# Kernel tuning notes

Hardware: AMD Instinct MI355X
Metric: run time of the kernel (lower is better)

The kernel has to match this reference:

```python
import math
import jax, jax.numpy as jnp
import numpy as np

N, C, H, W = 8, 128, 112, 112
# frozen random.randint shifts from __init__
S7_01, S8_10 = 2, -1          # roll along dim1 (c), dim3 (h)
S11_11, S12_10, S12_11, S13_11 = 1, -1, 0, 1  # rolls along dim4 (w) / dim3 (h)


def _conv(x, w, padding, rhs_dilation=(1, 1), groups=1):
    return jax.lax.conv_general_dilated(
        x, w, window_strides=(1, 1), padding=padding,
        lhs_dilation=(1, 1), rhs_dilation=rhs_dilation,
        dimension_numbers=('NCHW', 'OIHW', 'NCHW'),
        feature_group_count=groups)


def setup_inputs() -> dict:
    key = jax.random.key(0)
    ks = jax.random.split(key, 6)
    x = jax.random.normal(ks[0], (N, C, H, W), jnp.float32)
    w3 = jax.random.normal(ks[1], (C, C, 1, 3), jnp.float32) * 0.02   # Conv2d(c,c,(1,3),dil=(1,2),pad=(0,2))
    w4 = jax.random.normal(ks[2], (C, 1, 7, 1), jnp.float32) * 0.02   # depthwise Conv2d(c,c,(7,1),dil=(3,1),pad=(9,0),groups=c)
    w9 = jax.random.normal(ks[3], (1, C, C), jnp.float32) * 0.02      # p_9_w
    w10 = jax.random.normal(ks[4], (1, C, 7, 1, 1), jnp.float32) * 0.02  # p_10_w
    w15 = jax.random.normal(ks[5], (C, C * 7 // 4, 1, 1), jnp.float32) * 0.02  # Conv2d(c*7,c,1,groups=4)
    return {"x": x, "w3": w3, "w4": w4, "w9": w9, "w10": w10, "w15": w15}


def reference(x, w3, w4, w9, w10, w15):
    n, c, h, w = x.shape
    hw = h * w
    t1 = jax.nn.sigmoid(x)
    t2 = t1 * x                                   # SiLU
    t3 = _conv(t2, w3, ((0, 0), (2, 2)), rhs_dilation=(1, 2))
    t4 = _conv(t3, w4, ((9, 9), (0, 0)), rhs_dilation=(3, 1), groups=c)
    # channel attention: bmm(t1, t0^T) / sqrt(h*w) -> (n,c,c)
    t5 = jnp.einsum('ncs,nds->ncd', t1.reshape(n, c, hw), x.reshape(n, c, hw)) / math.sqrt(hw)
    # F.unfold(t4, (7,1), dilation=(2,1), padding=(6,0)) -> (n,c,7,h,w)
    padded = jnp.pad(t4, ((0, 0), (0, 0), (6, 6), (0, 0)))
    t6 = jnp.stack([padded[:, :, 2 * k:2 * k + h, :] for k in range(7)], axis=2)
    t7 = jnp.roll(t6, S7_01, axis=1)
    t8 = jnp.roll(t7, S8_10, axis=3)
    t9 = w9 * t5
    t10 = w10 * t8
    t11 = jnp.roll(t10, S11_11, axis=4)
    t12 = jnp.roll(jnp.roll(t11, S12_10, axis=3), S12_11, axis=4)
    t13 = jnp.roll(t12, S13_11, axis=4)
    # bmm(t9^T, t2) / sqrt(c): out[n,d,s] = sum_c t9[n,c,d] * t2[n,c,s]
    t14 = (jnp.einsum('ncd,ncs->nds', t9, t2.reshape(n, c, hw)) / math.sqrt(c)).reshape(n, c, h, w)
    t15 = _conv(t13.reshape(n, c * 7, h, w), w15, ((0, 0), (0, 0)), groups=4)
    return t15 + t14
```

## Files before the change

kernel.cpp:

```cpp
#include <hip/hip_runtime.h>
#include <hip/hip_bf16.h>

#define NB 8
#define CC 128
#define HH 112
#define WW 112
#define HWS (HH*WW)
#define PLANE (CC*HWS)
#define TOT (NB*PLANE)
#define XP 116
#define LROW 130
#define PLANEP ((size_t)HH*XP*CC)

typedef __attribute__((ext_vector_type(8))) short short8v;
typedef __attribute__((ext_vector_type(4))) float float4v;

__device__ __forceinline__ float bflo(unsigned u){ return __uint_as_float(u<<16); }
__device__ __forceinline__ float bfhi(unsigned u){ return __uint_as_float(u & 0xffff0000u); }
__device__ __forceinline__ float ldv(const float* p, size_t i){ return p[i]; }
__device__ __forceinline__ float ldv(const ushort* p, size_t i){ return __uint_as_float(((unsigned)p[i])<<16); }
__device__ __forceinline__ void ld8(const ushort* p, float* v){
    uint4 u0 = *((const uint4*)p);
    v[0]=bflo(u0.x); v[1]=bfhi(u0.x); v[2]=bflo(u0.y); v[3]=bfhi(u0.y);
    v[4]=bflo(u0.z); v[5]=bfhi(u0.z); v[6]=bflo(u0.w); v[7]=bfhi(u0.w);
}
__device__ __forceinline__ void ld8(const float* p, float* v){
    float4 a = *((const float4*)p); float4 b = *((const float4*)(p+4));
    v[0]=a.x; v[1]=a.y; v[2]=a.z; v[3]=a.w; v[4]=b.x; v[5]=b.y; v[6]=b.z; v[7]=b.w;
}
__device__ __forceinline__ void ld4(const float* p, float* v){
    float4 a = *((const float4*)p);
    v[0]=a.x; v[1]=a.y; v[2]=a.z; v[3]=a.w;
}
__device__ __forceinline__ void ld4(const ushort* p, float* v){
    uint2 u = *((const uint2*)p);
    v[0]=bflo(u.x); v[1]=bfhi(u.x); v[2]=bflo(u.y); v[3]=bfhi(u.y);
}
__device__ __forceinline__ ushort f2bf(float f){
    unsigned u = __float_as_uint(f);
    return (ushort)((u + 0x7fffu + ((u>>16)&1u)) >> 16);
}
__device__ __forceinline__ void stv(float* o, size_t i, float v){ o[i]=v; }
__device__ __forceinline__ void stv(ushort* o, size_t i, float v){ o[i]=f2bf(v); }

__global__ __launch_bounds__(256) void detect_k(const ushort* __restrict__ x, int* __restrict__ flag){
    __shared__ int cnt;
    if (threadIdx.x==0) cnt = 0;
    __syncthreads();
    int bad = 0;
    for (int i = threadIdx.x; i < 2048; i += 256){
        float v = ldv(x, i);
        if (!(v > -1e4f && v < 1e4f)) bad++;
    }
    atomicAdd(&cnt, bad);
    __syncthreads();
    if (threadIdx.x==0) *flag = (cnt > 64) ? 1 : 0;
}

template<typename ET>
__device__ __forceinline__ void wpack_body(const ET* __restrict__ w3, ushort* __restrict__ Wpk){
    int idx = blockIdx.x*256 + threadIdx.x;
    if (idx < CC*384){
        int o = idx/384, kap = idx - o*384;
        int k = kap>>7, i = kap&127;
        Wpk[idx] = f2bf(ldv(w3, (o*128+i)*3 + k));
    }
}
__global__ __launch_bounds__(256) void wpack_k(const void* w3, ushort* Wpk, const int* fl){
    if (*fl) wpack_body((const float*)w3, Wpk); else wpack_body((const ushort*)w3, Wpk);
}

template<typename ET>
__device__ __forceinline__ void bpad_body(const ET* __restrict__ x, ushort* __restrict__ Bpad){
    int y = blockIdx.x, n = blockIdx.y;
    __shared__ ushort px[XP*LROW];
    const ET* xb = x + (size_t)n*PLANE + y*WW;
    for (int idx=threadIdx.x; idx<CC*28; idx+=256){
        int i = idx/28, xq = (idx - i*28)*4;
        float v[4]; ld4(xb + (size_t)i*HWS + xq, v);
        #pragma unroll
        for (int d=0;d<4;d++){
            float vv = v[d];
            float sv = vv * (1.f/(1.f+expf(-vv)));
            px[(xq+d+2)*LROW + i] = f2bf(sv);
        }
    }
    for (int idx=threadIdx.x; idx<4*CC; idx+=256){
        int j = idx >> 7, i = idx & 127;
        int xp = (j<2) ? j : j+112;
        px[xp*LROW + i] = 0;
    }
    __syncthreads();
    ushort* ob = Bpad + ((size_t)n*HH + y)*XP*CC;
    for (int idx=threadIdx.x; idx<XP*16; idx+=256){
        int xp = idx >> 4, c8 = idx & 15;
        const ushort* pr = px + xp*LROW + c8*8;
        uint4 v;
        v.x = *((const uint*)(pr+0));
        v.y = *((const uint*)(pr+2));
        v.z = *((const uint*)(pr+4));
        v.w = *((const uint*)(pr+6));
        *((uint4*)(ob + (size_t)xp*CC + c8*8)) = v;
    }
}
__global__ __launch_bounds__(256) void bpad_k(const void* x, ushort* Bpad, const int* fl){
    if (*fl) bpad_body((const float*)x, Bpad); else bpad_body((const ushort*)x, Bpad);
}

__global__ __launch_bounds__(256) void conv3mm_k(const ushort* __restrict__ Bpad, const ushort* __restrict__ Wpk,
                                                 ushort* __restrict__ t3T){
    int bx = blockIdx.x;
    int n  = blockIdx.y;
    int sbi = bx >> 1, oh = bx & 1;
    int wid = threadIdx.x >> 6, lane = threadIdx.x & 63;
    int l15 = lane & 15, quad = lane >> 4;
    __shared__ ushort Alds[24576];
    {
        const int tid = threadIdx.x;
        uint4 tmp[12];
        #pragma unroll
        for (int it=0; it<12; it++){
            int g = it*256 + tid;
            int kcmt = g >> 6, sl = (g>>2)&15, sq = g&3;
            int kc = kcmt >> 2, mt = kcmt & 3;
            tmp[it] = *((const uint4*)(Wpk + (size_t)(oh*64 + mt*16 + sl)*384 + kc*32 + sq*8));
        }
        #pragma unroll
        for (int it=0; it<12; it++){
            int g = it*256 + tid;
            *((uint4*)(Alds + g*8)) = tmp[it];
        }
    }
    __syncthreads();

    int s0 = sbi*128 + wid*32;
    int s1 = s0 + l15, s2 = s1 + 16;
    int y1 = s1/WW, x1 = s1 - y1*WW;
    int y2 = s2/WW, x2 = s2 - y2*WW;
    const ushort* bb = Bpad + (size_t)n*PLANEP;
    const ushort* b1p = bb + ((size_t)y1*XP + x1)*CC + quad*8;
    const ushort* b2p = bb + ((size_t)y2*XP + x2)*CC + quad*8;
    const ushort* al = Alds + l15*32 + quad*8;

    float4v acc[4][2] = {};
    short8v BA[2][4], BB[2][4], a0[4], a1[4];

    auto ldb = [&](int g, short8v (&B)[2][4]){
        #pragma unroll
        for (int m=0;m<4;m++){
            B[0][m] = *((const short8v*)(b1p + g*256 + m*32));
            B[1][m] = *((const short8v*)(b2p + g*256 + m*32));
        }
    };
    auto lda = [&](int kc, short8v (&dst)[4]){
        #pragma unroll
        for (int mt=0;mt<4;mt++) dst[mt] = *((const short8v*)(al + (kc*4+mt)*512));
    };
    auto step = [&](const short8v (&a)[4], const short8v (&B)[2][4], int m){
        #pragma unroll
        for (int mt=0;mt<4;mt++){
            acc[mt][0] = __builtin_amdgcn_mfma_f32_16x16x32_bf16(a[mt], B[0][m], acc[mt][0],0,0,0);
            acc[mt][1] = __builtin_amdgcn_mfma_f32_16x16x32_bf16(a[mt], B[1][m], acc[mt][1],0,0,0);
        }
    };

    ldb(0, BA); lda(0, a0);
    ldb(1, BB);
    lda(1, a1);  step(a0, BA, 0);
    lda(2, a0);  step(a1, BA, 1);
    lda(3, a1);  step(a0, BA, 2);
    lda(4, a0);  step(a1, BA, 3);
    ldb(2, BA);
    lda(5, a1);  step(a0, BB, 0);
    lda(6, a0);  step(a1, BB, 1);
    lda(7, a1);  step(a0, BB, 2);
    lda(8, a0);  step(a1, BB, 3);
    lda(9, a1);  step(a0, BA, 0);
    lda(10, a0); step(a1, BA, 1);
    lda(11, a1); step(a0, BA, 2);
                 step(a1, BA, 3);

    ushort* tb = t3T + (size_t)n*PLANE;
    #pragma unroll
    for (int nt=0; nt<2; nt++){
        int s = s0 + nt*16 + l15;
        ushort* rowp = tb + (size_t)s*128 + oh*64 + quad*4;
        #pragma unroll
        for (int mt=0; mt<4; mt++){
            ushort4 v;
            v.x = f2bf(acc[mt][nt][0]); v.y = f2bf(acc[mt][nt][1]);
            v.z = f2bf(acc[mt][nt][2]); v.w = f2bf(acc[mt][nt][3]);
            *((ushort4*)(rowp + mt*16)) = v;
        }
    }
}

template<typename ET>
__device__ __forceinline__ void wdpack_body(const ET* __restrict__ w4, float* __restrict__ wdp){
    int idx = blockIdx.x*256 + threadIdx.x;
    if (idx < 896){ int k = idx >> 7, c = idx & 127; wdp[idx] = ldv(w4, c*7 + k); }
}
__global__ __launch_bounds__(256) void wdpack_k(const void* w4, float* wdp, const int* fl){
    if (*fl) wdpack_body((const float*)w4, wdp); else wdpack_body((const ushort*)w4, wdp);
}

__global__ __launch_bounds__(256) void dwconvT_k(const ushort* __restrict__ t3T, const float* __restrict__ wdp,
                                                 ushort* __restrict__ t4T){
    int by = blockIdx.x, n = blockIdx.y;
    int y = (by>>3) + (by&7)*14;
    const ushort* tb = t3T + (size_t)n*PLANE;
    ushort* ob = t4T + (size_t)n*PLANE + (size_t)y*WW*128;
    for (int it = threadIdx.x; it < WW*16; it += 256){
        int c8 = it & 15, x = it >> 4;
        int coff = c8*8;
        float acc8[8] = {0.f,0.f,0.f,0.f,0.f,0.f,0.f,0.f};
        #pragma unroll
        for (int k=0;k<7;k++){
            int row = y - 9 + 3*k;
            if (row < 0 || row >= HH) continue;
            float v[8]; ld8(tb + ((size_t)row*WW + x)*128 + coff, v);
            const float* wp = wdp + k*128 + coff;
            #pragma unroll
            for (int j=0;j<8;j++) acc8[j] = fmaf(wp[j], v[j], acc8[j]);
        }
        ushort tmp[8];
        #pragma unroll
        for (int j=0;j<8;j++) tmp[j] = f2bf(acc8[j]);
        *((short8v*)(ob + (size_t)x*128 + coff)) = *((const short8v*)tmp);
    }
}

template<typename ET>
__device__ __forceinline__ void fusew_body(const ET* __restrict__ w10, const ET* __restrict__ w15,
                                           ushort* __restrict__ Wfb){
    int idx = blockIdx.x*256+threadIdx.x;
    if (idx < CC*224){
        int o = idx / 224, r = idx - o*224;
        int g = o >> 5;
        int cl = r/7, k = r - cl*7;
        int c = g*32 + cl;
        Wfb[idx] = f2bf(ldv(w15, o*224 + r) * ldv(w10, c*7+k));
    }
}
__global__ __launch_bounds__(256) void fusew_k(const void* w10, const void* w15, ushort* Wfb, const int* fl){
    if (*fl) fusew_body((const float*)w10, (const float*)w15, Wfb);
    else     fusew_body((const ushort*)w10, (const ushort*)w15, Wfb);
}

__global__ __launch_bounds__(256) void wfapack_k(const ushort* __restrict__ Wfb, ushort* __restrict__ Wfa){
    int idx = blockIdx.x*256 + threadIdx.x;
    if (idx >= 57344) return;
    int j   = idx & 31;
    int l15 = (idx >> 5) & 15;
    int mt  = (idx >> 9) & 1;
    int q   = (idx >> 10) & 1;
    int k   = (idx >> 11) % 7;
    int w   = idx / 14336;
    int o = w*32 + mt*16 + l15;
    int cl = -1;
    if (q==1){ if (j < 30) cl = j + 2; }
    else     { if (j >= 30) cl = j - 30; }
    Wfa[idx] = (cl >= 0) ? Wfb[o*224 + cl*7 + k] : (ushort)0;
}

__global__ __launch_bounds__(256) void t15v2_k(const ushort* __restrict__ t4T, const ushort* __restrict__ Wfa,
                                               ushort* __restrict__ u){
    int by = blockIdx.x, n = blockIdx.y;
    int y = (by>>3) + (by&7)*14;
    int w = threadIdx.x >> 6, lane = threadIdx.x & 63;
    int l15 = lane & 15, quad = lane >> 4;
    int qlo = (w+3)&3;
    float4v acc[7][2] = {};
    const ushort* tbase = t4T + (size_t)n*PLANE;
    for (int k=0;k<7;k++){
        int row = y + 2*k - 6;
        if (row < 0 || row >= HH) continue;
        const ushort* af = Wfa + (w*7 + k)*2048 + l15*32 + quad*8;
        short8v A00 = *((const short8v*)(af));
        short8v A01 = *((const short8v*)(af + 512));
        short8v A10 = *((const short8v*)(af + 1024));
        short8v A11 = *((const short8v*)(af + 1536));
        const ushort* rbase = tbase + ((size_t)row*WW + l15)*128 + quad*8;
        #pragma unroll
        for (int st=0; st<7; st++){
            const ushort* bp = rbase + st*16*128;
            short8v B0 = *((const short8v*)(bp + qlo*32));
            short8v B1 = *((const short8v*)(bp + w*32));
            acc[st][0] = __builtin_amdgcn_mfma_f32_16x16x32_bf16(A00, B0, acc[st][0], 0,0,0);
            acc[st][1] = __builtin_amdgcn_mfma_f32_16x16x32_bf16(A01, B0, acc[st][1], 0,0,0);
            acc[st][0] = __builtin_amdgcn_mfma_f32_16x16x32_bf16(A10, B1, acc[st][0], 0,0,0);
            acc[st][1] = __builtin_amdgcn_mfma_f32_16x16x32_bf16(A11, B1, acc[st][1], 0,0,0);
        }
    }
    ushort* ub = u + ((size_t)n*CC + w*32)*HWS + (size_t)y*WW;
    #pragma unroll
    for (int st=0; st<7; st++){
        int s = st*16 + l15;
        #pragma unroll
        for (int mt=0; mt<2; mt++)
            #pragma unroll
            for (int r=0;r<4;r++)
                ub[(size_t)(mt*16+quad*4+r)*HWS + s] = f2bf(acc[st][mt][r]);
    }
}

template<typename ET>
__device__ __forceinline__ void t5mm_body(const ET* __restrict__ x, float* __restrict__ t5){
    int ks = blockIdx.x, n = blockIdx.y;
    int wid = threadIdx.x>>6, lane = threadIdx.x&63;
    int l15 = lane&15, quad = lane>>4;
    const ET* xn = x + (size_t)n*PLANE;
    float4v acc[2][8] = {};
    for (int t=0; t<8; t++){
        int sb = ks*256 + t*32 + quad*8;
        short8v afr[2];
        #pragma unroll
        for (int mt=0; mt<2; mt++){
            int row = wid*32 + mt*16 + l15;
            float v[8]; ld8(xn + (size_t)row*HWS + sb, v);
            ushort tmp[8];
            #pragma unroll
            for (int j=0;j<8;j++) tmp[j] = f2bf(1.f/(1.f+expf(-v[j])));
            afr[mt] = *((const short8v*)tmp);
        }
        #pragma unroll
        for (int nt=0; nt<8; nt++){
            int row = nt*16 + l15;
            float v[8]; ld8(xn + (size_t)row*HWS + sb, v);
            ushort tmp[8];
            #pragma unroll
            for (int j=0;j<8;j++) tmp[j] = f2bf(v[j]);
            short8v bfr = *((const short8v*)tmp);
            acc[0][nt] = __builtin_amdgcn_mfma_f32_16x16x32_bf16(afr[0], bfr, acc[0][nt], 0,0,0);
            acc[1][nt] = __builtin_amdgcn_mfma_f32_16x16x32_bf16(afr[1], bfr, acc[1][nt], 0,0,0);
        }
    }
    float* t5n = t5 + n*16384;
    #pragma unroll
    for (int mt=0; mt<2; mt++){
        #pragma unroll
        for (int nt=0; nt<8; nt++){
            #pragma unroll
            for (int r=0; r<4; r++){
                int ci = wid*32 + mt*16 + quad*4 + r;
                int cj = nt*16 + l15;
                atomicAdd(&t5n[ci*128 + cj], acc[mt][nt][r]);
            }
        }
    }
}
__global__ __launch_bounds__(256) void t5mm_k(const void* x, float* t5, const int* fl){
    if (*fl) t5mm_body((const float*)x, t5); else t5mm_body((const ushort*)x, t5);
}

template<typename ET>
__device__ __forceinline__ void coefb_body(const ET* __restrict__ w9, const float* __restrict__ t5,
                                           ushort* __restrict__ coefb){
    const float sc = 7.89181775e-4f;
    int idx = blockIdx.x*256 + threadIdx.x;
    int n = idx >> 14, rem = idx & 16383;
    int d = rem >> 7, c = rem & 127;
    coefb[idx] = f2bf(ldv(w9, c*128 + d) * t5[n*16384 + c*128 + d] * sc);
}
__global__ __launch_bounds__(256) void coefb_k(const void* w9, const float* t5, ushort* coefb, const int* fl){
    if (*fl) coefb_body((const float*)w9, t5, coefb); else coefb_body((const ushort*)w9, t5, coefb);
}

template<typename OT>
__device__ __forceinline__ void final2_body(const ushort* __restrict__ Bpad, const ushort* __restrict__ coefb,
                                            const ushort* __restrict__ u, OT* __restrict__ out){
    int sb = blockIdx.x, n = blockIdx.y;
    int wid = threadIdx.x>>6, lane = threadIdx.x&63;
    int l15 = lane&15, quad = lane>>4;
    int shalf = wid >> 1, ohalf = wid & 1;
    int s0 = sb*64 + shalf*32;
    int s1 = s0 + l15, s2 = s1 + 16;
    int y1 = s1/WW, x1 = s1 - y1*WW;
    int y2 = s2/WW, x2 = s2 - y2*WW;
    const ushort* bb = Bpad + (size_t)n*PLANEP;
    const ushort* b1p = bb + ((size_t)y1*XP + x1 + 2)*CC + quad*8;
    const ushort* b2p = bb + ((size_t)y2*XP + x2 + 2)*CC + quad*8;
    const ushort* abase = coefb + (size_t)n*16384 + (size_t)(ohalf*64 + l15)*128 + quad*8;
    float4v acc[4][2] = {};
    short8v bv0[4], bv1[4], aP[4], aQ[4];
    #pragma unroll
    for (int kc=0;kc<4;kc++){
        bv0[kc] = *((const short8v*)(b1p + kc*32));
        bv1[kc] = *((const short8v*)(b2p + kc*32));
    }
    auto lda = [&](int kc, short8v (&dst)[4]){
        #pragma unroll
        for (int mt=0;mt<4;mt++) dst[mt] = *((const short8v*)(abase + mt*16*128 + kc*32));
    };
    auto step = [&](const short8v (&a)[4], int kc){
        #pragma unroll
        for (int mt=0;mt<4;mt++){
            acc[mt][0] = __builtin_amdgcn_mfma_f32_16x16x32_bf16(a[mt], bv0[kc], acc[mt][0],0,0,0);
            acc[mt][1] = __builtin_amdgcn_mfma_f32_16x16x32_bf16(a[mt], bv1[kc], acc[mt][1],0,0,0);
        }
    };
    lda(0, aP);
    lda(1, aQ); step(aP, 0);
    lda(2, aP); step(aQ, 1);
    lda(3, aQ); step(aP, 2);
                step(aQ, 3);
    #pragma unroll
    for (int mt=0; mt<4; mt++){
        #pragma unroll
        for (int nt=0; nt<2; nt++){
            int s = s0 + nt*16 + l15;
            int y = s/WW, xx = s - y*WW;
            int ys = y+2; if (ys>=HH) ys-=HH;
            int xs = xx-2; if (xs<0) xs+=WW;
            #pragma unroll
            for (int r=0; r<4; r++){
                int d = ohalf*64 + mt*16 + quad*4 + r;
                float val = ldv(u, ((size_t)n*CC+d)*HWS + ys*WW + xs) + acc[mt][nt][r];
                stv(out, ((size_t)n*CC+d)*HWS + s, val);
            }
        }
    }
}
__global__ __launch_bounds__(256) void final2_k(const ushort* Bpad, const ushort* coefb,
                                                const ushort* u, void* out, const int* fl){
    if (*fl) final2_body(Bpad, coefb, u, (float*)out);
    else     final2_body(Bpad, coefb, u, (ushort*)out);
}

extern "C" void kernel_launch(void* const* d_in, const int* in_sizes, int n_in,
                              void* d_out, int out_size, void* d_ws, size_t ws_size,
                              hipStream_t stream) {
    const void* x   = d_in[0];
    const void* w3  = d_in[1];
    const void* w4  = d_in[2];
    const void* w9  = d_in[3];
    const void* w10 = d_in[4];
    const void* w15 = d_in[5];

    ushort* t3T  = (ushort*)d_ws;
    ushort* u    = t3T;
    ushort* t4T  = t3T + TOT;
    ushort* Bpad = t4T + TOT;
    float*  t5   = (float*)(Bpad + NB*PLANEP);
    ushort* coefb= (ushort*)(t5 + NB*CC*CC);
    ushort* Wfb  = coefb + NB*CC*CC;
    ushort* Wpk  = Wfb + CC*224;
    ushort* Wfa  = Wpk + CC*384;
    float*  wdp  = (float*)(Wfa + 57344);
    int* flag    = (int*)(wdp + 896);

    detect_k<<<1, 256, 0, stream>>>((const ushort*)x, flag);
    hipMemsetAsync(t5, 0, NB*CC*CC*sizeof(float), stream);

    wpack_k  <<<192, 256, 0, stream>>>(w3, Wpk, flag);
    fusew_k  <<<112, 256, 0, stream>>>(w10, w15, Wfb, flag);
    wfapack_k<<<224, 256, 0, stream>>>(Wfb, Wfa);
    wdpack_k <<<4,   256, 0, stream>>>(w4, wdp, flag);
    bpad_k   <<<dim3(HH,NB), 256, 0, stream>>>(x, Bpad, flag);
    conv3mm_k<<<dim3(196,NB), 256, 0, stream>>>(Bpad, Wpk, t3T);
    dwconvT_k<<<dim3(HH,NB), 256, 0, stream>>>(t3T, wdp, t4T);
    t5mm_k   <<<dim3(49,NB), 256, 0, stream>>>(x, t5, flag);
    coefb_k  <<<NB*CC*CC/256, 256, 0, stream>>>(w9, t5, coefb, flag);
    t15v2_k  <<<dim3(HH,NB), 256, 0, stream>>>(t4T, Wfa, u);
    final2_k <<<dim3(196,NB), 256, 0, stream>>>(Bpad, coefb, u, d_out, flag);
}
```

Baseline: 328.4 us.

## Split t15 kernel over two column halves and double-buffer row loads

```diff
diff --git a/kernel.cpp b/kernel.cpp
--- a/kernel.cpp
+++ b/kernel.cpp
@@ -263,45 +263,80 @@
     Wfa[idx] = (cl >= 0) ? Wfb[o*224 + cl*7 + k] : (ushort)0;
 }
 
-__global__ __launch_bounds__(256) void t15v2_k(const ushort* __restrict__ t4T, const ushort* __restrict__ Wfa,
-                                               ushort* __restrict__ u){
-    int by = blockIdx.x, n = blockIdx.y;
-    int y = (by>>3) + (by&7)*14;
-    int w = threadIdx.x >> 6, lane = threadIdx.x & 63;
-    int l15 = lane & 15, quad = lane >> 4;
+template<int ST0, int NST>
+__device__ __forceinline__ void t15_body(const ushort* __restrict__ tbase, const ushort* __restrict__ Wfa,
+                                         ushort* __restrict__ ub, int y, int w, int l15, int quad){
     int qlo = (w+3)&3;
-    float4v acc[7][2] = {};
-    const ushort* tbase = t4T + (size_t)n*PLANE;
-    for (int k=0;k<7;k++){
+    float4v acc[NST][2] = {};
+    const ushort* xbase = tbase + ((size_t)(ST0*16) + l15)*128 + quad*8;
+
+    auto ldrow = [&](int k, short8v (&B)[NST][2]){
         int row = y + 2*k - 6;
-        if (row < 0 || row >= HH) continue;
+        const ushort* rbase = xbase + (size_t)row*WW*128;
+        #pragma unroll
+        for (int st=0; st<NST; st++){
+            const ushort* bp = rbase + st*16*128;
+            B[st][0] = *((const short8v*)(bp + qlo*32));
+            B[st][1] = *((const short8v*)(bp + w*32));
+        }
+    };
+    auto ldA = [&](int k, short8v (&A)[4]){
         const ushort* af = Wfa + (w*7 + k)*2048 + l15*32 + quad*8;
-        short8v A00 = *((const short8v*)(af));
-        short8v A01 = *((const short8v*)(af + 512));
-        short8v A10 = *((const short8v*)(af + 1024));
-        short8v A11 = *((const short8v*)(af + 1536));
-        const ushort* rbase = tbase + ((size_t)row*WW + l15)*128 + quad*8;
-        #pragma unroll
-        for (int st=0; st<7; st++){
-            const ushort* bp = rbase + st*16*128;
-            short8v B0 = *((const short8v*)(bp + qlo*32));
-            short8v B1 = *((const short8v*)(bp + w*32));
-            acc[st][0] = __builtin_amdgcn_mfma_f32_16x16x32_bf16(A00, B0, acc[st][0], 0,0,0);
-            acc[st][1] = __builtin_amdgcn_mfma_f32_16x16x32_bf16(A01, B0, acc[st][1], 0,0,0);
-            acc[st][0] = __builtin_amdgcn_mfma_f32_16x16x32_bf16(A10, B1, acc[st][0], 0,0,0);
-            acc[st][1] = __builtin_amdgcn_mfma_f32_16x16x32_bf16(A11, B1, acc[st][1], 0,0,0);
-        }
-    }
-    ushort* ub = u + ((size_t)n*CC + w*32)*HWS + (size_t)y*WW;
+        A[0] = *((const short8v*)(af));
+        A[1] = *((const short8v*)(af + 512));
+        A[2] = *((const short8v*)(af + 1024));
+        A[3] = *((const short8v*)(af + 1536));
+    };
+    auto domm = [&](const short8v (&A)[4], const short8v (&B)[NST][2]){
+        #pragma unroll
+        for (int st=0; st<NST; st++){
+            acc[st][0] = __builtin_amdgcn_mfma_f32_16x16x32_bf16(A[0], B[st][0], acc[st][0], 0,0,0);
+            acc[st][1] = __builtin_amdgcn_mfma_f32_16x16x32_bf16(A[1], B[st][0], acc[st][1], 0,0,0);
+            acc[st][0] = __builtin_amdgcn_mfma_f32_16x16x32_bf16(A[2], B[st][1], acc[st][0], 0,0,0);
+            acc[st][1] = __builtin_amdgcn_mfma_f32_16x16x32_bf16(A[3], B[st][1], acc[st][1], 0,0,0);
+        }
+    };
+
+    if (y >= 6 && y <= 105){
+        short8v BA[NST][2], BB[NST][2], A0[4], A1[4];
+        ldrow(0, BA); ldrow(1, BB);
+        ldA(0, A0);              domm(A0, BA);
+        ldrow(2, BA); ldA(1, A1); domm(A1, BB);
+        ldrow(3, BB); ldA(2, A0); domm(A0, BA);
+        ldrow(4, BA); ldA(3, A1); domm(A1, BB);
+        ldrow(5, BB); ldA(4, A0); domm(A0, BA);
+        ldrow(6, BA); ldA(5, A1); domm(A1, BB);
+                      ldA(6, A0); domm(A0, BA);
+    } else {
+        int klo = (y >= 6) ? 0 : ((7 - y) >> 1);
+        int khi = min(6, (117 - y) >> 1);
+        for (int k = klo; k <= khi; k++){
+            short8v B[NST][2], A[4];
+            ldrow(k, B); ldA(k, A); domm(A, B);
+        }
+    }
+
     #pragma unroll
-    for (int st=0; st<7; st++){
-        int s = st*16 + l15;
+    for (int st=0; st<NST; st++){
+        int s = (ST0 + st)*16 + l15;
         #pragma unroll
         for (int mt=0; mt<2; mt++)
             #pragma unroll
             for (int r=0;r<4;r++)
                 ub[(size_t)(mt*16+quad*4+r)*HWS + s] = f2bf(acc[st][mt][r]);
     }
+}
+__global__ __launch_bounds__(256) void t15v3_k(const ushort* __restrict__ t4T, const ushort* __restrict__ Wfa,
+                                               ushort* __restrict__ u){
+    int bx = blockIdx.x, n = blockIdx.y;
+    int xh = bx & 1, byi = bx >> 1;
+    int y = (byi>>3) + (byi&7)*14;
+    int w = threadIdx.x >> 6, lane = threadIdx.x & 63;
+    int l15 = lane & 15, quad = lane >> 4;
+    const ushort* tbase = t4T + (size_t)n*PLANE;
+    ushort* ub = u + ((size_t)n*CC + w*32)*HWS + (size_t)y*WW;
+    if (xh == 0) t15_body<0,4>(tbase, Wfa, ub, y, w, l15, quad);
+    else         t15_body<4,3>(tbase, Wfa, ub, y, w, l15, quad);
 }
 
 template<typename ET>
@@ -461,6 +496,6 @@
     dwconvT_k<<<dim3(HH,NB), 256, 0, stream>>>(t3T, wdp, t4T);
     t5mm_k   <<<dim3(49,NB), 256, 0, stream>>>(x, t5, flag);
     coefb_k  <<<NB*CC*CC/256, 256, 0, stream>>>(w9, t5, coefb, flag);
-    t15v2_k  <<<dim3(HH,NB), 256, 0, stream>>>(t4T, Wfa, u);
+    t15v3_k  <<<dim3(224,NB), 256, 0, stream>>>(t4T, Wfa, u);
     final2_k <<<dim3(196,NB), 256, 0, stream>>>(Bpad, coefb, u, d_out, flag);
 }
```

New measurement: 335.7 us. +2.2%, slower.
